# Optimization experiments

Hardware: AMD Instinct MI355X
Metric: run time of the kernel (lower is better)

Reference implementation:

```python
import jax, jax.numpy as jnp
import numpy as np

N, E, D = 50000, 600000, 128
NEG_SLOPE = 0.2

def setup_inputs() -> dict:
    key = jax.random.key(0)
    ks = jax.random.split(key, 12)
    s = 1.0 / np.sqrt(D)
    return {
        "x": jax.random.normal(ks[0], (N, D), jnp.float32),
        "edge_index": jax.random.randint(ks[1], (2, E), 0, N),
        "edge_attr": jax.random.normal(ks[2], (E, D), jnp.float32),
        "ln1_g": jnp.ones((D,), jnp.float32),
        "ln1_b": jnp.zeros((D,), jnp.float32),
        "W_lin": jax.random.normal(ks[3], (D, D), jnp.float32) * s,
        "att_src": jax.random.normal(ks[4], (D,), jnp.float32) * s,
        "att_dst": jax.random.normal(ks[5], (D,), jnp.float32) * s,
        "W_edge": jax.random.normal(ks[6], (D, D), jnp.float32) * s,
        "att_edge": jax.random.normal(ks[7], (D,), jnp.float32) * s,
        "gat_bias": jnp.zeros((D,), jnp.float32),
        "ln2_g": jnp.ones((D,), jnp.float32),
        "ln2_b": jnp.zeros((D,), jnp.float32),
        "W1": jax.random.normal(ks[8], (D, 4 * D), jnp.float32) * s,
        "b1": jnp.zeros((4 * D,), jnp.float32),
        "W2": jax.random.normal(ks[9], (4 * D, D), jnp.float32) * (1.0 / np.sqrt(4 * D)),
        "b2": jnp.zeros((D,), jnp.float32),
    }


def _layernorm(x, g, b, eps=1e-5):
    mu = jnp.mean(x, axis=-1, keepdims=True)
    var = jnp.mean(jnp.square(x - mu), axis=-1, keepdims=True)
    return (x - mu) * jax.lax.rsqrt(var + eps) * g + b


def _gat_conv(x, edge_index, edge_attr, W_lin, att_src, att_dst, W_edge, att_edge, gat_bias):
    # PyG GATConv, heads=1, concat=False, add_self_loops=False, edge_dim=D
    src, dst = edge_index[0], edge_index[1]
    h = x @ W_lin                      # [N, D] shared src/dst projection
    a_src = h @ att_src                # [N]
    a_dst = h @ att_dst                # [N]
    a_edge = (edge_attr @ W_edge) @ att_edge  # [E]
    alpha = a_src[src] + a_dst[dst] + a_edge  # [E]
    alpha = jnp.where(alpha > 0, alpha, NEG_SLOPE * alpha)  # leaky_relu(0.2)
    # segment softmax over destination nodes
    m = jax.ops.segment_max(alpha, dst, num_segments=N)
    m = jnp.where(jnp.isfinite(m), m, 0.0)
    ex = jnp.exp(alpha - m[dst])
    denom = jax.ops.segment_sum(ex, dst, num_segments=N)
    coef = ex / jnp.maximum(denom[dst], 1e-16)
    # weighted scatter-aggregation of source messages
    out = jax.ops.segment_sum(coef[:, None] * h[src], dst, num_segments=N)
    return out + gat_bias


def reference(x, edge_index, edge_attr, ln1_g, ln1_b, W_lin, att_src, att_dst,
              W_edge, att_edge, gat_bias, ln2_g, ln2_b, W1, b1, W2, b2):
    # pre-norm + GAT message passing + residual (dropout = eval identity)
    xn = _layernorm(x, ln1_g, ln1_b)
    x = x + _gat_conv(xn, edge_index, edge_attr, W_lin, att_src, att_dst,
                      W_edge, att_edge, gat_bias)
    # pre-norm + FFN + residual
    xn = _layernorm(x, ln2_g, ln2_b)
    ffn = jax.nn.relu(xn @ W1 + b1) @ W2 + b2
    return x + ffn
```

## Files before the change

### kernel.cpp

```cpp
#include <hip/hip_runtime.h>

#define D 128
#define NEG_SLOPE 0.2f

typedef __attribute__((ext_vector_type(8))) short short8;
typedef __attribute__((ext_vector_type(4))) float f32x4;

__device__ __forceinline__ float wred_sum(float v){
#pragma unroll
  for (int m = 32; m; m >>= 1) v += __shfl_xor(v, m);
  return v;
}
__device__ __forceinline__ int wred_sumi(int v){
#pragma unroll
  for (int m = 32; m; m >>= 1) v += __shfl_xor(v, m);
  return v;
}
__device__ __forceinline__ float wred_max(float v){
#pragma unroll
  for (int m = 32; m; m >>= 1) v = fmaxf(v, __shfl_xor(v, m));
  return v;
}
__device__ __forceinline__ unsigned short bf16r(float f){
  unsigned int u = __float_as_uint(f);
  u += 0x7fffu + ((u >> 16) & 1u);
  return (unsigned short)(u >> 16);
}
__device__ __forceinline__ float bf2f(unsigned int hi16){
  return __uint_as_float(hi16 << 16);
}

__global__ void k_prep0(const float* __restrict__ W_lin, const float* __restrict__ W1,
                        const float* __restrict__ W2, const float* __restrict__ W_edge,
                        const float* __restrict__ att_edge,
                        unsigned short* __restrict__ Wlt, unsigned short* __restrict__ W1t,
                        unsigned short* __restrict__ W2t, float* __restrict__ we,
                        int* __restrict__ cnt, int N){
  int t = blockIdx.x * blockDim.x + threadIdx.x;
  if (t < N) cnt[t] = 0;
  if (t < 128 * 128){
    int c = t >> 7, k = t & 127;
    Wlt[t] = bf16r(W_lin[k * 128 + c]);
  } else if (t < 128 * 128 + 512 * 128){
    int u = t - 128 * 128; int c = u >> 7, k = u & 127;
    W1t[u] = bf16r(W1[k * 512 + c]);
  } else if (t < 128 * 128 + 512 * 128 + 128 * 512){
    int u = t - (128 * 128 + 512 * 128); int c = u >> 9, k = u & 511;
    W2t[u] = bf16r(W2[k * 128 + c]);
  } else {
    int u = t - (128 * 128 + 512 * 128 + 128 * 512);
    if (u < 128){
      float s = 0.f;
      for (int j = 0; j < 128; ++j) s += W_edge[u * 128 + j] * att_edge[j];
      we[u] = s;
    }
  }
}

__global__ __launch_bounds__(256) void k_hgemm(const float* __restrict__ x,
                                               const unsigned short* __restrict__ Wlt,
                                               const float* __restrict__ ln1_g,
                                               const float* __restrict__ ln1_b,
                                               const float* __restrict__ att_src,
                                               const float* __restrict__ att_dst,
                                               const int* __restrict__ ei,
                                               unsigned short* __restrict__ hq,
                                               float* __restrict__ asrc,
                                               float* __restrict__ adst,
                                               int* __restrict__ cnt, int N, int E){
  __shared__ unsigned short wbuf[16384];
#pragma unroll
  for (int r = 0; r < 8; ++r){
    int idx = r * 256 + threadIdx.x;
    int c = idx >> 4, kc = idx & 15;
    short8 w = *(const short8*)(Wlt + c * 128 + kc * 8);
    *(short8*)((char*)wbuf + c * 256 + ((kc * 16) ^ ((c & 7) << 4))) = w;
  }
  __syncthreads();
  int wid = threadIdx.x >> 6, lane = threadIdx.x & 63;
  int rb = blockIdx.x * 64 + wid * 16;
  int row = rb + (lane & 15);
  int rowc = row < N ? row : N - 1;
  int ksub = (lane >> 4) * 8;
  float v[4][8];
#pragma unroll
  for (int kb = 0; kb < 4; ++kb){
    float4 p0 = *(const float4*)(x + (size_t)rowc * 128 + kb * 32 + ksub);
    float4 p1 = *(const float4*)(x + (size_t)rowc * 128 + kb * 32 + ksub + 4);
    v[kb][0]=p0.x; v[kb][1]=p0.y; v[kb][2]=p0.z; v[kb][3]=p0.w;
    v[kb][4]=p1.x; v[kb][5]=p1.y; v[kb][6]=p1.z; v[kb][7]=p1.w;
  }
  float s = 0.f;
#pragma unroll
  for (int kb = 0; kb < 4; ++kb)
#pragma unroll
    for (int j = 0; j < 8; ++j) s += v[kb][j];
  s += __shfl_xor(s, 16); s += __shfl_xor(s, 32);
  float mu = s * (1.0f / 128.f);
  float q = 0.f;
#pragma unroll
  for (int kb = 0; kb < 4; ++kb)
#pragma unroll
    for (int j = 0; j < 8; ++j){ float d = v[kb][j] - mu; q += d * d; }
  q += __shfl_xor(q, 16); q += __shfl_xor(q, 32);
  float rstd = rsqrtf(q * (1.0f / 128.f) + 1e-5f);
  short8 a[4];
#pragma unroll
  for (int kb = 0; kb < 4; ++kb){
    float4 g0 = *(const float4*)(ln1_g + kb * 32 + ksub);
    float4 g1 = *(const float4*)(ln1_g + kb * 32 + ksub + 4);
    float4 b0 = *(const float4*)(ln1_b + kb * 32 + ksub);
    float4 b1 = *(const float4*)(ln1_b + kb * 32 + ksub + 4);
    float gg[8] = {g0.x,g0.y,g0.z,g0.w,g1.x,g1.y,g1.z,g1.w};
    float bb[8] = {b0.x,b0.y,b0.z,b0.w,b1.x,b1.y,b1.z,b1.w};
#pragma unroll
    for (int j = 0; j < 8; ++j)
      a[kb][j] = (short)bf16r((v[kb][j] - mu) * rstd * gg[j] + bb[j]);
  }
  f32x4 acc[8];
#pragma unroll
  for (int ct = 0; ct < 8; ++ct) acc[ct] = (f32x4){0.f, 0.f, 0.f, 0.f};
#pragma unroll
  for (int ct = 0; ct < 8; ++ct){
    int col = ct * 16 + (lane & 15);
    int cswz = (col & 7) << 4;
#pragma unroll
    for (int kb = 0; kb < 4; ++kb){
      short8 bf = *(const short8*)((const char*)wbuf + col * 256 +
                                   ((kb * 64 + ksub * 2) ^ cswz));
      acc[ct] = __builtin_amdgcn_mfma_f32_16x16x32_bf16(a[kb], bf, acc[ct], 0, 0, 0);
    }
  }
  int r0 = rb + (lane >> 4) * 4;
#pragma unroll
  for (int ct = 0; ct < 8; ++ct){
    int col = ct * 16 + (lane & 15);
#pragma unroll
    for (int j = 0; j < 4; ++j){
      int r = r0 + j;
      if (r < N) hq[(size_t)r * 128 + col] = bf16r(acc[ct][j]);
    }
  }
  float as_v[8], ad_v[8];
#pragma unroll
  for (int ct = 0; ct < 8; ++ct){
    int col = ct * 16 + (lane & 15);
    as_v[ct] = att_src[col];
    ad_v[ct] = att_dst[col];
  }
  float ps[4] = {0.f,0.f,0.f,0.f}, pd[4] = {0.f,0.f,0.f,0.f};
#pragma unroll
  for (int ct = 0; ct < 8; ++ct)
#pragma unroll
    for (int j = 0; j < 4; ++j){
      ps[j] += acc[ct][j] * as_v[ct];
      pd[j] += acc[ct][j] * ad_v[ct];
    }
#pragma unroll
  for (int m = 1; m < 16; m <<= 1)
#pragma unroll
    for (int j = 0; j < 4; ++j){
      ps[j] += __shfl_xor(ps[j], m);
      pd[j] += __shfl_xor(pd[j], m);
    }
  if ((lane & 15) == 0){
#pragma unroll
    for (int j = 0; j < 4; ++j){
      int r = r0 + j;
      if (r < N){ asrc[r] = ps[j]; adst[r] = pd[j]; }
    }
  }
  int t = blockIdx.x * blockDim.x + threadIdx.x;
  int stride = gridDim.x * blockDim.x;
  for (int e = t; e < E; e += stride) atomicAdd(&cnt[ei[E + e]], 1);
}

__global__ void k_escan(const int* __restrict__ cnt, int* __restrict__ start,
                        int* __restrict__ cursor, int N){
  int b = blockIdx.x, t = threadIdx.x;
  int base = b * 256;
  int acc = 0;
  for (int i = t; i < base; i += 256) acc += cnt[i];
  acc = wred_sumi(acc);
  __shared__ int wsum[4];
  if ((t & 63) == 0) wsum[t >> 6] = acc;
  __syncthreads();
  int s_off = wsum[0] + wsum[1] + wsum[2] + wsum[3];
  int i = base + t;
  int c = (i < N) ? cnt[i] : 0;
  __shared__ int sd[256];
  sd[t] = c;
  __syncthreads();
  for (int off = 1; off < 256; off <<= 1){
    int vv = (t >= off) ? sd[t - off] : 0;
    __syncthreads();
    sd[t] += vv;
    __syncthreads();
  }
  int st = s_off + sd[t] - c;
  if (i <= N) start[i] = st;
  if (i < N) cursor[i] = st;
}

__global__ void k_edge_scatter(const float* __restrict__ ea, const int* __restrict__ ei,
                               const float* __restrict__ we, const float* __restrict__ asrc,
                               const float* __restrict__ adst, int* __restrict__ cursor,
                               int2* __restrict__ esa, int E){
  int gw = (blockIdx.x * blockDim.x + threadIdx.x) >> 6;
  int lane = threadIdx.x & 63;
  int e = gw * 2 + (lane >> 5);
  int li = lane & 31;
  if (e >= E) return;
  float4 v = *(const float4*)(ea + (size_t)e * 128 + li * 4);
  float4 w = *(const float4*)(we + li * 4);
  float s = v.x * w.x + v.y * w.y + v.z * w.z + v.w * w.w;
#pragma unroll
  for (int m = 16; m; m >>= 1) s += __shfl_xor(s, m);
  if (li == 0){
    int sn = ei[e], dn = ei[E + e];
    float al = asrc[sn] + adst[dn] + s;
    al = al > 0.f ? al : NEG_SLOPE * al;
    int slot = atomicAdd(&cursor[dn], 1);
    esa[slot] = make_int2(sn, __float_as_int(al));
  }
}

__global__ void k_agg(const float* __restrict__ x, const unsigned short* __restrict__ hq,
                      const int* __restrict__ start, const int2* __restrict__ esa,
                      const float* __restrict__ gat_bias,
                      const float* __restrict__ g2, const float* __restrict__ b2,
                      float* __restrict__ out, unsigned short* __restrict__ xn2q, int N){
  int n = (blockIdx.x * blockDim.x + threadIdx.x) >> 6;
  int lane = threadIdx.x & 63;
  if (n >= N) return;
  int beg = start[n], end = start[n + 1];
  float m = -1e30f;
  for (int i = beg + lane; i < end; i += 64) m = fmaxf(m, __int_as_float(esa[i].y));
  m = wred_max(m);
  float ds = 0.f, a0 = 0.f, a1 = 0.f;
#pragma unroll 2
  for (int s = beg; s < end; ++s){
    int2 ev = esa[s];
    float ex = __expf(__int_as_float(ev.y) - m);
    ds += ex;
    unsigned int hv = *(const unsigned int*)(hq + (size_t)ev.x * 128 + lane * 2);
    a0 += ex * bf2f(hv & 0xffffu);
    a1 += ex * bf2f(hv >> 16);
  }
  float inv = (end > beg) ? 1.f / fmaxf(ds, 1e-16f) : 0.f;
  a0 *= inv; a1 *= inv;
  float2 xv  = *(const float2*)(x + (size_t)n * 128 + lane * 2);
  float2 gbv = *(const float2*)(gat_bias + lane * 2);
  float r0 = xv.x + a0 + gbv.x;
  float r1 = xv.y + a1 + gbv.y;
  float mu = wred_sum(r0 + r1) * (1.0f / 128.f);
  float d0 = r0 - mu, d1 = r1 - mu;
  float var = wred_sum(d0 * d0 + d1 * d1) * (1.0f / 128.f);
  float rstd = rsqrtf(var + 1e-5f);
  float2 gv = *(const float2*)(g2 + lane * 2);
  float2 bv = *(const float2*)(b2 + lane * 2);
  float o0 = d0 * rstd * gv.x + bv.x;
  float o1 = d1 * rstd * gv.y + bv.y;
  *(float2*)(out + (size_t)n * 128 + lane * 2) = make_float2(r0, r1);
  unsigned int pk = (unsigned int)bf16r(o0) | ((unsigned int)bf16r(o1) << 16);
  *(unsigned int*)(xn2q + (size_t)n * 128 + lane * 2) = pk;
}

__global__ __launch_bounds__(1024, 8) void k_ffn(const unsigned short* __restrict__ xn2q,
                                                 const unsigned short* __restrict__ W1t,
                                                 const unsigned short* __restrict__ W2t,
                                                 const float* __restrict__ b1,
                                                 const float* __restrict__ b2,
                                                 float* __restrict__ out, int N){
  __shared__ unsigned short hid[64 * 512];
  int wid = threadIdx.x >> 6, lane = threadIdx.x & 63;
  int rg = wid >> 2;
  int cq = wid & 3;
  int i = lane & 15, g = lane >> 4;
  int ksub = g * 8;
  int rb = blockIdx.x * 64;
  int arow = rb + rg * 16 + i;
  int arowc = arow < N ? arow : N - 1;
  short8 a[4];
#pragma unroll
  for (int kb = 0; kb < 4; ++kb)
    a[kb] = *(const short8*)(xn2q + (size_t)arowc * 128 + kb * 32 + ksub);
  int lr0 = rg * 16 + g * 4;
#pragma unroll
  for (int ct = 0; ct < 8; ++ct){
    int col = cq * 128 + ct * 16 + i;
    f32x4 acc = {0.f, 0.f, 0.f, 0.f};
#pragma unroll
    for (int kb = 0; kb < 4; ++kb){
      short8 bf = *(const short8*)(W1t + (size_t)col * 128 + kb * 32 + ksub);
      acc = __builtin_amdgcn_mfma_f32_16x16x32_bf16(a[kb], bf, acc, 0, 0, 0);
    }
    float bias = b1[col];
#pragma unroll
    for (int j = 0; j < 4; ++j){
      float v = acc[j] + bias;
      v = v > 0.f ? v : 0.f;
      int row = lr0 + j;
      int byte = (col * 2) ^ ((row & 7) << 4);
      *(unsigned short*)((char*)hid + row * 1024 + byte) = bf16r(v);
    }
  }
  __syncthreads();
  f32x4 acc2[2];
  acc2[0] = (f32x4){0.f, 0.f, 0.f, 0.f};
  acc2[1] = (f32x4){0.f, 0.f, 0.f, 0.f};
  int arow2 = rg * 16 + i;
#pragma unroll 4
  for (int kb = 0; kb < 16; ++kb){
    int kbyte = (kb * 32 + ksub) * 2;
    int sb = kbyte ^ ((arow2 & 7) << 4);
    short8 af = *(const short8*)((const char*)hid + arow2 * 1024 + sb);
#pragma unroll
    for (int u = 0; u < 2; ++u){
      int col = (cq * 2 + u) * 16 + i;
      short8 bf = *(const short8*)(W2t + (size_t)col * 512 + kb * 32 + ksub);
      acc2[u] = __builtin_amdgcn_mfma_f32_16x16x32_bf16(af, bf, acc2[u], 0, 0, 0);
    }
  }
  int r0 = rb + lr0;
#pragma unroll
  for (int u = 0; u < 2; ++u){
    int col = (cq * 2 + u) * 16 + i;
    float bias = b2[col];
#pragma unroll
    for (int j = 0; j < 4; ++j){
      int row = r0 + j;
      if (row < N) out[(size_t)row * 128 + col] += acc2[u][j] + bias;
    }
  }
}

extern "C" void kernel_launch(void* const* d_in, const int* in_sizes, int n_in,
                              void* d_out, int out_size, void* d_ws, size_t ws_size,
                              hipStream_t stream){
  const float* x        = (const float*)d_in[0];
  const int*   ei       = (const int*)  d_in[1];
  const float* ea       = (const float*)d_in[2];
  const float* ln1_g    = (const float*)d_in[3];
  const float* ln1_b    = (const float*)d_in[4];
  const float* W_lin    = (const float*)d_in[5];
  const float* att_src  = (const float*)d_in[6];
  const float* att_dst  = (const float*)d_in[7];
  const float* W_edge   = (const float*)d_in[8];
  const float* att_edge = (const float*)d_in[9];
  const float* gat_bias = (const float*)d_in[10];
  const float* ln2_g    = (const float*)d_in[11];
  const float* ln2_b    = (const float*)d_in[12];
  const float* W1       = (const float*)d_in[13];
  const float* b1       = (const float*)d_in[14];
  const float* W2       = (const float*)d_in[15];
  const float* b2       = (const float*)d_in[16];

  const int N = in_sizes[0] / 128;
  const int E = in_sizes[2] / 128;
  float* out = (float*)d_out;

  char* pp = (char*)d_ws;
  auto carve = [&](size_t bytes) -> char* {
    char* r = pp; pp += (bytes + 255) & ~(size_t)255; return r;
  };
  unsigned short* hq     = (unsigned short*)carve((size_t)N * 128 * 2);
  unsigned short* xn2q   = (unsigned short*)carve((size_t)N * 128 * 2);
  float*          asrc   = (float*)carve((size_t)N * 4);
  float*          adst   = (float*)carve((size_t)N * 4);
  int2*           esa    = (int2*)carve((size_t)E * 8);
  int*            cnt    = (int*)carve((size_t)N * 4);
  int*            cursor = (int*)carve((size_t)N * 4);
  int*            start  = (int*)carve((size_t)(N + 1) * 4);
  unsigned short* Wlt    = (unsigned short*)carve(128 * 128 * 2);
  unsigned short* W1t    = (unsigned short*)carve(512 * 128 * 2);
  unsigned short* W2t    = (unsigned short*)carve(128 * 512 * 2);
  float*          we     = (float*)carve(128 * 4);

  k_prep0<<<(128*128 + 512*128 + 128*512 + 128 + 255) / 256, 256, 0, stream>>>(
      W_lin, W1, W2, W_edge, att_edge, Wlt, W1t, W2t, we, cnt, N);
  k_hgemm<<<(N + 63) / 64, 256, 0, stream>>>(x, Wlt, ln1_g, ln1_b, att_src, att_dst, ei,
                                             hq, asrc, adst, cnt, N, E);
  k_escan<<<N / 256 + 1, 256, 0, stream>>>(cnt, start, cursor, N);
  k_edge_scatter<<<(E + 7) / 8, 256, 0, stream>>>(ea, ei, we, asrc, adst, cursor, esa, E);
  k_agg<<<(N + 3) / 4, 256, 0, stream>>>(x, hq, start, esa, gat_bias, ln2_g, ln2_b,
                                         out, xn2q, N);
  k_ffn<<<(N + 63) / 64, 1024, 0, stream>>>(xn2q, W1t, W2t, b1, b2, out, N);
}
```

Before: 350.3 us.

## Split FFN into two persistent kernels with LDS-resident weights

Replaces the fused FFN kernel, which kept the hidden activations in LDS and streamed weights from global memory per tile, with two persistent kernels. Each kernel loads its full bf16 weight matrix (128 KB) into swizzled LDS once and loops over row tiles. The hidden activations (N x 512 bf16) now round-trip through global memory. This removes repeated global weight loads, at the cost of extra HBM traffic, an additional launch and one block per CU because of the LDS footprint.

```diff
diff --git a/kernel.cpp b/kernel.cpp
--- a/kernel.cpp
+++ b/kernel.cpp
@@ -266,71 +266,96 @@
   *(unsigned int*)(xn2q + (size_t)n * 128 + lane * 2) = pk;
 }
 
-__global__ __launch_bounds__(1024, 8) void k_ffn(const unsigned short* __restrict__ xn2q,
-                                                 const unsigned short* __restrict__ W1t,
-                                                 const unsigned short* __restrict__ W2t,
-                                                 const float* __restrict__ b1,
-                                                 const float* __restrict__ b2,
-                                                 float* __restrict__ out, int N){
-  __shared__ unsigned short hid[64 * 512];
+__global__ __launch_bounds__(1024) void k_ffn1(const unsigned short* __restrict__ xn2q,
+                                               const unsigned short* __restrict__ W1t,
+                                               const float* __restrict__ b1,
+                                               unsigned short* __restrict__ hid, int N){
+  __shared__ unsigned short wlds[512 * 128];
+#pragma unroll
+  for (int r = 0; r < 8; ++r){
+    int idx = r * 1024 + threadIdx.x;
+    int c = idx >> 4, kc = idx & 15;
+    short8 w = *(const short8*)(W1t + c * 128 + kc * 8);
+    *(short8*)((char*)wlds + c * 256 + ((kc * 16) ^ ((c & 7) << 4))) = w;
+  }
+  __syncthreads();
   int wid = threadIdx.x >> 6, lane = threadIdx.x & 63;
-  int rg = wid >> 2;
-  int cq = wid & 3;
   int i = lane & 15, g = lane >> 4;
-  int ksub = g * 8;
-  int rb = blockIdx.x * 64;
-  int arow = rb + rg * 16 + i;
-  int arowc = arow < N ? arow : N - 1;
-  short8 a[4];
-#pragma unroll
-  for (int kb = 0; kb < 4; ++kb)
-    a[kb] = *(const short8*)(xn2q + (size_t)arowc * 128 + kb * 32 + ksub);
-  int lr0 = rg * 16 + g * 4;
-#pragma unroll
-  for (int ct = 0; ct < 8; ++ct){
-    int col = cq * 128 + ct * 16 + i;
-    f32x4 acc = {0.f, 0.f, 0.f, 0.f};
-#pragma unroll
-    for (int kb = 0; kb < 4; ++kb){
-      short8 bf = *(const short8*)(W1t + (size_t)col * 128 + kb * 32 + ksub);
-      acc = __builtin_amdgcn_mfma_f32_16x16x32_bf16(a[kb], bf, acc, 0, 0, 0);
-    }
-    float bias = b1[col];
-#pragma unroll
-    for (int j = 0; j < 4; ++j){
-      float v = acc[j] + bias;
-      v = v > 0.f ? v : 0.f;
-      int row = lr0 + j;
-      int byte = (col * 2) ^ ((row & 7) << 4);
-      *(unsigned short*)((char*)hid + row * 1024 + byte) = bf16r(v);
-    }
+  int T = (N + 63) >> 6;
+  for (int t = blockIdx.x; t < T; t += gridDim.x){
+    int rb = t * 64;
+#pragma unroll 1
+    for (int sub = 0; sub < 4; ++sub){
+      int arow = rb + sub * 16 + i;
+      int arowc = arow < N ? arow : N - 1;
+      short8 a[4];
+#pragma unroll
+      for (int kb = 0; kb < 4; ++kb)
+        a[kb] = *(const short8*)(xn2q + (size_t)arowc * 128 + kb * 32 + g * 8);
+#pragma unroll
+      for (int u = 0; u < 2; ++u){
+        int col = (wid * 2 + u) * 16 + i;
+        int cswz = (col & 7) << 4;
+        f32x4 acc = {0.f, 0.f, 0.f, 0.f};
+#pragma unroll
+        for (int kb = 0; kb < 4; ++kb){
+          short8 bf = *(const short8*)((const char*)wlds + col * 256 +
+                                       ((kb * 64 + g * 16) ^ cswz));
+          acc = __builtin_amdgcn_mfma_f32_16x16x32_bf16(a[kb], bf, acc, 0, 0, 0);
+        }
+        float bias = b1[col];
+#pragma unroll
+        for (int j = 0; j < 4; ++j){
+          float v = acc[j] + bias;
+          v = v > 0.f ? v : 0.f;
+          int orow = rb + sub * 16 + g * 4 + j;
+          if (orow < N) hid[(size_t)orow * 512 + col] = bf16r(v);
+        }
+      }
+    }
+  }
+}
+
+__global__ __launch_bounds__(1024) void k_ffn2(const unsigned short* __restrict__ hid,
+                                               const unsigned short* __restrict__ W2t,
+                                               const float* __restrict__ b2,
+                                               float* __restrict__ out, int N){
+  __shared__ unsigned short wlds[128 * 512];
+#pragma unroll
+  for (int r = 0; r < 8; ++r){
+    int idx = r * 1024 + threadIdx.x;
+    int c = idx >> 6, kc = idx & 63;
+    short8 w = *(const short8*)(W2t + c * 512 + kc * 8);
+    *(short8*)((char*)wlds + c * 1024 + ((kc * 16) ^ ((c & 7) << 4))) = w;
   }
   __syncthreads();
-  f32x4 acc2[2];
-  acc2[0] = (f32x4){0.f, 0.f, 0.f, 0.f};
-  acc2[1] = (f32x4){0.f, 0.f, 0.f, 0.f};
-  int arow2 = rg * 16 + i;
+  int wid = threadIdx.x >> 6, lane = threadIdx.x & 63;
+  int i = lane & 15, g = lane >> 4;
+  int cs = wid & 7, rh = wid >> 3;
+  int col = cs * 16 + i;
+  int cswz = (col & 7) << 4;
+  float bias = b2[col];
+  int T = (N + 63) >> 6;
+  for (int t = blockIdx.x; t < T; t += gridDim.x){
+    int rb = t * 64;
+#pragma unroll 1
+    for (int sub = 0; sub < 2; ++sub){
+      int r16 = rb + rh * 32 + sub * 16;
+      int arow = r16 + i;
+      int arowc = arow < N ? arow : N - 1;
+      f32x4 acc = {0.f, 0.f, 0.f, 0.f};
 #pragma unroll 4
-  for (int kb = 0; kb < 16; ++kb){
-    int kbyte = (kb * 32 + ksub) * 2;
-    int sb = kbyte ^ ((arow2 & 7) << 4);
-    short8 af = *(const short8*)((const char*)hid + arow2 * 1024 + sb);
-#pragma unroll
-    for (int u = 0; u < 2; ++u){
-      int col = (cq * 2 + u) * 16 + i;
-      short8 bf = *(const short8*)(W2t + (size_t)col * 512 + kb * 32 + ksub);
-      acc2[u] = __builtin_amdgcn_mfma_f32_16x16x32_bf16(af, bf, acc2[u], 0, 0, 0);
-    }
-  }
-  int r0 = rb + lr0;
-#pragma unroll
-  for (int u = 0; u < 2; ++u){
-    int col = (cq * 2 + u) * 16 + i;
-    float bias = b2[col];
-#pragma unroll
-    for (int j = 0; j < 4; ++j){
-      int row = r0 + j;
-      if (row < N) out[(size_t)row * 128 + col] += acc2[u][j] + bias;
+      for (int kb = 0; kb < 16; ++kb){
+        short8 af = *(const short8*)(hid + (size_t)arowc * 512 + kb * 32 + g * 8);
+        short8 bf = *(const short8*)((const char*)wlds + col * 1024 +
+                                     ((kb * 64 + g * 16) ^ cswz));
+        acc = __builtin_amdgcn_mfma_f32_16x16x32_bf16(af, bf, acc, 0, 0, 0);
+      }
+#pragma unroll
+      for (int j = 0; j < 4; ++j){
+        int row = r16 + g * 4 + j;
+        if (row < N) out[(size_t)row * 128 + col] += acc[j] + bias;
+      }
     }
   }
 }
@@ -366,6 +391,7 @@
   };
   unsigned short* hq     = (unsigned short*)carve((size_t)N * 128 * 2);
   unsigned short* xn2q   = (unsigned short*)carve((size_t)N * 128 * 2);
+  unsigned short* hid    = (unsigned short*)carve((size_t)N * 512 * 2);
   float*          asrc   = (float*)carve((size_t)N * 4);
   float*          adst   = (float*)carve((size_t)N * 4);
   int2*           esa    = (int2*)carve((size_t)E * 8);
@@ -385,5 +411,6 @@
   k_edge_scatter<<<(E + 7) / 8, 256, 0, stream>>>(ea, ei, we, asrc, adst, cursor, esa, E);
   k_agg<<<(N + 3) / 4, 256, 0, stream>>>(x, hq, start, esa, gat_bias, ln2_g, ln2_b,
                                          out, xn2q, N);
-  k_ffn<<<(N + 63) / 64, 1024, 0, stream>>>(xn2q, W1t, W2t, b1, b2, out, N);
-}
+  k_ffn1<<<256, 1024, 0, stream>>>(xn2q, W1t, b1, hid, N);
+  k_ffn2<<<256, 1024, 0, stream>>>(hid, W2t, b2, out, N);
+}
```

New measurement: 329.5 us. 1.06x faster.

## Chunk FFN hidden dim and stage weight slices in LDS across two row tiles

Applied to the files above, without the earlier changes.

Rewrites the FFN kernel to process the 512-wide hidden layer in four 128-wide chunks. Each chunk's W1 and W2 slices are staged into swizzled shared memory and reused for two 64-row tiles per block, with the second GEMM accumulated in registers. A fixed 512-block grid with 512 threads replaces one 1024-thread block per tile. This aims to cut repeated global/L2 weight fetches and shrink the hidden LDS buffer, at the cost of more barriers and serialized chunk loops.

```diff
diff --git a/kernel.cpp b/kernel.cpp
--- a/kernel.cpp
+++ b/kernel.cpp
@@ -266,71 +266,104 @@
   *(unsigned int*)(xn2q + (size_t)n * 128 + lane * 2) = pk;
 }
 
-__global__ __launch_bounds__(1024, 8) void k_ffn(const unsigned short* __restrict__ xn2q,
-                                                 const unsigned short* __restrict__ W1t,
-                                                 const unsigned short* __restrict__ W2t,
-                                                 const float* __restrict__ b1,
-                                                 const float* __restrict__ b2,
-                                                 float* __restrict__ out, int N){
-  __shared__ unsigned short hid[64 * 512];
-  int wid = threadIdx.x >> 6, lane = threadIdx.x & 63;
-  int rg = wid >> 2;
-  int cq = wid & 3;
+__global__ __launch_bounds__(512) void k_ffn(const unsigned short* __restrict__ xn2q,
+                                             const unsigned short* __restrict__ W1t,
+                                             const unsigned short* __restrict__ W2t,
+                                             const float* __restrict__ b1,
+                                             const float* __restrict__ b2,
+                                             float* __restrict__ out, int N, int T){
+  __shared__ unsigned short w1lds[128 * 128];
+  __shared__ unsigned short w2lds[128 * 128];
+  __shared__ unsigned short hid[64 * 128];
+  int tid = threadIdx.x;
+  int wid = tid >> 6, lane = tid & 63;
+  int rg = wid >> 1, ch = wid & 1;
   int i = lane & 15, g = lane >> 4;
-  int ksub = g * 8;
-  int rb = blockIdx.x * 64;
-  int arow = rb + rg * 16 + i;
-  int arowc = arow < N ? arow : N - 1;
-  short8 a[4];
-#pragma unroll
-  for (int kb = 0; kb < 4; ++kb)
-    a[kb] = *(const short8*)(xn2q + (size_t)arowc * 128 + kb * 32 + ksub);
-  int lr0 = rg * 16 + g * 4;
-#pragma unroll
-  for (int ct = 0; ct < 8; ++ct){
-    int col = cq * 128 + ct * 16 + i;
-    f32x4 acc = {0.f, 0.f, 0.f, 0.f};
-#pragma unroll
-    for (int kb = 0; kb < 4; ++kb){
-      short8 bf = *(const short8*)(W1t + (size_t)col * 128 + kb * 32 + ksub);
-      acc = __builtin_amdgcn_mfma_f32_16x16x32_bf16(a[kb], bf, acc, 0, 0, 0);
-    }
-    float bias = b1[col];
-#pragma unroll
-    for (int j = 0; j < 4; ++j){
-      float v = acc[j] + bias;
-      v = v > 0.f ? v : 0.f;
-      int row = lr0 + j;
-      int byte = (col * 2) ^ ((row & 7) << 4);
-      *(unsigned short*)((char*)hid + row * 1024 + byte) = bf16r(v);
-    }
-  }
-  __syncthreads();
-  f32x4 acc2[2];
-  acc2[0] = (f32x4){0.f, 0.f, 0.f, 0.f};
-  acc2[1] = (f32x4){0.f, 0.f, 0.f, 0.f};
-  int arow2 = rg * 16 + i;
-#pragma unroll 4
-  for (int kb = 0; kb < 16; ++kb){
-    int kbyte = (kb * 32 + ksub) * 2;
-    int sb = kbyte ^ ((arow2 & 7) << 4);
-    short8 af = *(const short8*)((const char*)hid + arow2 * 1024 + sb);
-#pragma unroll
+  int t0 = blockIdx.x, t1 = blockIdx.x + gridDim.x;
+  short8 a[2][4];
+#pragma unroll
+  for (int u = 0; u < 2; ++u){
+    int t = u ? t1 : t0;
+    if (t < T){
+      int arow = t * 64 + rg * 16 + i;
+      int arowc = arow < N ? arow : N - 1;
+#pragma unroll
+      for (int kb = 0; kb < 4; ++kb)
+        a[u][kb] = *(const short8*)(xn2q + (size_t)arowc * 128 + kb * 32 + g * 8);
+    }
+  }
+  f32x4 acc[2][4];
+#pragma unroll
+  for (int u = 0; u < 2; ++u)
+#pragma unroll
+    for (int ct = 0; ct < 4; ++ct) acc[u][ct] = (f32x4){0.f, 0.f, 0.f, 0.f};
+#pragma unroll 1
+  for (int c = 0; c < 4; ++c){
+#pragma unroll
+    for (int qq = 0; qq < 4; ++qq){
+      int idx = qq * 512 + tid;
+      int cl = idx >> 4, kc = idx & 15;
+      int dst = cl * 256 + ((kc * 16) ^ ((cl & 7) << 4));
+      short8 w1v = *(const short8*)(W1t + (size_t)(c * 128 + cl) * 128 + kc * 8);
+      *(short8*)((char*)w1lds + dst) = w1v;
+      short8 w2v = *(const short8*)(W2t + (size_t)cl * 512 + c * 128 + kc * 8);
+      *(short8*)((char*)w2lds + dst) = w2v;
+    }
+    __syncthreads();
+#pragma unroll 1
     for (int u = 0; u < 2; ++u){
-      int col = (cq * 2 + u) * 16 + i;
-      short8 bf = *(const short8*)(W2t + (size_t)col * 512 + kb * 32 + ksub);
-      acc2[u] = __builtin_amdgcn_mfma_f32_16x16x32_bf16(af, bf, acc2[u], 0, 0, 0);
-    }
-  }
-  int r0 = rb + lr0;
+      int t = u ? t1 : t0;
+      if (t >= T) break;
+#pragma unroll
+      for (int ct = 0; ct < 4; ++ct){
+        int hcol = ch * 64 + ct * 16 + i;
+        int cswz = (hcol & 7) << 4;
+        f32x4 hacc = {0.f, 0.f, 0.f, 0.f};
+#pragma unroll
+        for (int kb = 0; kb < 4; ++kb){
+          short8 bf = *(const short8*)((const char*)w1lds + hcol * 256 +
+                                       ((kb * 64 + g * 16) ^ cswz));
+          hacc = __builtin_amdgcn_mfma_f32_16x16x32_bf16(a[u][kb], bf, hacc, 0, 0, 0);
+        }
+        float bias = b1[c * 128 + hcol];
+#pragma unroll
+        for (int j = 0; j < 4; ++j){
+          float v = hacc[j] + bias;
+          v = v > 0.f ? v : 0.f;
+          int nl = rg * 16 + g * 4 + j;
+          *(unsigned short*)((char*)hid + nl * 256 + ((hcol * 2) ^ ((nl & 7) << 4))) = bf16r(v);
+        }
+      }
+      __syncthreads();
+#pragma unroll
+      for (int kbl = 0; kbl < 4; ++kbl){
+        int nrow = rg * 16 + i;
+        short8 af = *(const short8*)((const char*)hid + nrow * 256 +
+                                     ((kbl * 64 + g * 16) ^ ((nrow & 7) << 4)));
+#pragma unroll
+        for (int ct = 0; ct < 4; ++ct){
+          int ocol = ch * 64 + ct * 16 + i;
+          short8 bf = *(const short8*)((const char*)w2lds + ocol * 256 +
+                                       ((kbl * 64 + g * 16) ^ ((ocol & 7) << 4)));
+          acc[u][ct] = __builtin_amdgcn_mfma_f32_16x16x32_bf16(af, bf, acc[u][ct], 0, 0, 0);
+        }
+      }
+      __syncthreads();
+    }
+  }
 #pragma unroll
   for (int u = 0; u < 2; ++u){
-    int col = (cq * 2 + u) * 16 + i;
-    float bias = b2[col];
-#pragma unroll
-    for (int j = 0; j < 4; ++j){
-      int row = r0 + j;
-      if (row < N) out[(size_t)row * 128 + col] += acc2[u][j] + bias;
+    int t = u ? t1 : t0;
+    if (t >= T) break;
+#pragma unroll
+    for (int ct = 0; ct < 4; ++ct){
+      int ocol = ch * 64 + ct * 16 + i;
+      float bias = b2[ocol];
+#pragma unroll
+      for (int j = 0; j < 4; ++j){
+        int row = t * 64 + rg * 16 + g * 4 + j;
+        if (row < N) out[(size_t)row * 128 + ocol] += acc[u][ct][j] + bias;
+      }
     }
   }
 }
@@ -358,6 +391,7 @@
 
   const int N = in_sizes[0] / 128;
   const int E = in_sizes[2] / 128;
+  const int T = (N + 63) / 64;
   float* out = (float*)d_out;
 
   char* pp = (char*)d_ws;
@@ -385,5 +419,5 @@
   k_edge_scatter<<<(E + 7) / 8, 256, 0, stream>>>(ea, ei, we, asrc, adst, cursor, esa, E);
   k_agg<<<(N + 3) / 4, 256, 0, stream>>>(x, hq, start, esa, gat_bias, ln2_g, ln2_b,
                                          out, xn2q, N);
-  k_ffn<<<(N + 63) / 64, 1024, 0, stream>>>(xn2q, W1t, W2t, b1, b2, out, N);
-}
+  k_ffn<<<512, 512, 0, stream>>>(xn2q, W1t, W2t, b1, b2, out, N, T);
+}
```

Result: faster. 331.3 us (-5.4%).
